# Kernel tuning notes

Measured on AMD Instinct MI355X. Metric: run time of the kernel, lower is better.

## Reference

```python
import jax, jax.numpy as jnp
import numpy as np

N = 8192      # atoms
B = 64        # molecules
E = 262144    # edges
S = 4         # species
NMAX = 8      # radial basis size
CUT = 5.0     # cutoff radius
AVG_ATOMS = 128.0
E_SCALE = 1.0
PS_DIM = (S * NMAX) ** 2 * 4  # l_max=3 -> 4 l channels -> 4096
H1, H2 = 1024, 1024
OUT = 1


def _sph_harm(u):
    # real spherical harmonics up to l=3, input unit vectors [E,3] -> [E,16]
    x, y, z = u[:, 0], u[:, 1], u[:, 2]
    x2, y2, z2 = x * x, y * y, z * z
    return jnp.stack([
        0.28209479 * jnp.ones_like(x),
        0.48860251 * y, 0.48860251 * z, 0.48860251 * x,
        1.09254843 * x * y, 1.09254843 * y * z, 0.31539157 * (3.0 * z2 - 1.0),
        1.09254843 * x * z, 0.54627422 * (x2 - y2),
        0.59004359 * y * (3.0 * x2 - y2), 2.89061144 * x * y * z,
        0.45704579 * y * (5.0 * z2 - 1.0), 0.37317633 * z * (5.0 * z2 - 3.0),
        0.45704579 * x * (5.0 * z2 - 1.0), 1.44530572 * z * (x2 - y2),
        0.59004359 * x * (x2 - 3.0 * y2),
    ], axis=-1)


def setup_inputs() -> dict:
    key = jax.random.key(0)
    ks = jax.random.split(key, 12)
    positions = jax.random.normal(ks[0], (N, 3), dtype=jnp.float32) * 1.5  # dense cloud so many pairs < CUT
    cells = jnp.tile(20.0 * jnp.eye(3, dtype=jnp.float32)[None], (B, 1, 1))
    numbers = jax.random.randint(ks[1], (N,), 0, S)
    edge_indices = jax.random.randint(ks[2], (2, E), 0, N)
    edge_offsets = jnp.zeros((E, 3), dtype=jnp.float32)
    batch = jnp.arange(N) // (N // B)
    gamma = 1.0 + 0.1 * jax.random.normal(ks[3], (PS_DIM,), dtype=jnp.float32)
    beta = 0.1 * jax.random.normal(ks[4], (PS_DIM,), dtype=jnp.float32)
    W_ps = jax.random.normal(ks[5], (PS_DIM, OUT), dtype=jnp.float32) / np.sqrt(PS_DIM)
    W1 = jax.random.normal(ks[6], (PS_DIM, H1), dtype=jnp.float32) / np.sqrt(PS_DIM)
    W2 = jax.random.normal(ks[7], (H1, H2), dtype=jnp.float32) / np.sqrt(H1)
    W3 = jax.random.normal(ks[8], (H2, OUT), dtype=jnp.float32) / np.sqrt(H2)
    W_comp = jax.random.normal(ks[9], (S, OUT), dtype=jnp.float32) / np.sqrt(S)
    return dict(positions=positions, cells=cells, numbers=numbers,
                edge_indices=edge_indices, edge_offsets=edge_offsets, batch=batch,
                gamma=gamma, beta=beta, W_ps=W_ps, W1=W1, W2=W2, W3=W3, W_comp=W_comp)


def reference(positions, cells, numbers, edge_indices, edge_offsets, batch,
              gamma, beta, W_ps, W1, W2, W3, W_comp):
    i, j = edge_indices[0], edge_indices[1]  # center, neighbor
    # periodic shift: fractional offsets through the cell of the center's molecule
    shift = jnp.einsum('ec,ecd->ed', edge_offsets, cells[batch[i]])
    rvec = positions[j] - positions[i] + shift                      # [E,3]
    r = jnp.sqrt(jnp.sum(rvec * rvec, axis=-1) + 1e-12)             # [E]
    u = rvec / r[:, None]
    fc = 0.5 * (jnp.cos(jnp.pi * jnp.minimum(r, CUT) / CUT) + 1.0) * (r < CUT)
    n = jnp.arange(1, NMAX + 1, dtype=positions.dtype)
    R = fc[:, None] * jnp.sin(jnp.pi * n[None, :] * r[:, None] / CUT) / r[:, None]  # [E,NMAX]
    Y = _sph_harm(u)                                                # [E,16]
    edge_feat = R[:, :, None] * Y[:, None, :]                       # [E,NMAX,16]
    # spherical expansion c[i, species(j), n, lm] via scatter-add
    seg = i * S + numbers[j]
    c = jax.ops.segment_sum(edge_feat, seg, num_segments=N * S)     # [N*S,NMAX,16]
    c = c.reshape(N, S * NMAX, 16)
    # power spectrum: contract over m within each l block
    bounds = [(0, 1), (1, 4), (4, 9), (9, 16)]
    p = [jnp.einsum('ixm,iym->ixy', c[:, :, s:e], c[:, :, s:e]) for s, e in bounds]
    ps = jnp.stack(p, axis=-1).reshape(N, PS_DIM)                   # [N,4096]
    # LayerNorm (eps=1e-5, affine)
    mu = jnp.mean(ps, axis=-1, keepdims=True)
    var = jnp.var(ps, axis=-1, keepdims=True)
    psn = (ps - mu) / jnp.sqrt(var + 1e-5) * gamma + beta
    # linear branch + MLP branch
    psl = psn @ W_ps                                                # [N,1]
    h = jax.nn.silu(psn @ W1)
    h = jax.nn.silu(h @ W2)
    psnn = h @ W3                                                   # [N,1]
    # pool atomic energies into per-molecule totals (index_add)
    energies = jax.ops.segment_sum(psl + psnn, batch, num_segments=B) / AVG_ATOMS
    # eval path: composition baseline
    comp = jax.ops.segment_sum(jax.nn.one_hot(numbers, S, dtype=psn.dtype), batch, num_segments=B)
    return energies * E_SCALE + comp @ W_comp                       # [B,1]
```

## Files before the change

### kernel.cpp

```cpp
#include <hip/hip_runtime.h>
#include <hip/hip_bf16.h>
#include <math.h>

#define N_ATOMS 8192
#define B_BATCH 64
#define E_EDGES 262144
#define S_SPEC 4
#define NMAX 8
#define PS_DIM 4096
#define PS_K 2304
#define H1_DIM 1024
#define CAP4 48
#define CUTR 5.0f
#define PI_F 3.14159265358979f

typedef float floatx4 __attribute__((ext_vector_type(4)));
typedef int intx8 __attribute__((ext_vector_type(8)));
typedef unsigned char u8;

__device__ __forceinline__ void g2lds16(const void* g, void* l) {
    __builtin_amdgcn_global_load_lds(
        (const __attribute__((address_space(1))) void*)g,
        (__attribute__((address_space(3))) void*)l, 16, 0, 0);
}

__device__ __forceinline__ int pk_fp8x4(float a, float b, float c, float d) {
    int lo = __builtin_amdgcn_cvt_pk_fp8_f32(a, b, 0, false);
    return __builtin_amdgcn_cvt_pk_fp8_f32(c, d, lo, true);
}

__global__ __launch_bounds__(256) void prep_kernel(
    const float* __restrict__ pos, const float* __restrict__ cells,
    const int* __restrict__ numbers, const int* __restrict__ ei,
    const float* __restrict__ eo, const int* __restrict__ batch,
    int* __restrict__ cnt, float4* __restrict__ bucket,
    const float* __restrict__ W1, const float* __restrict__ gamma,
    const float* __restrict__ beta, const float* __restrict__ Wps,
    const float* __restrict__ W2,
    u8* __restrict__ Wt1, u8* __restrict__ Wt2, float* __restrict__ b1,
    float* __restrict__ gw, float* __restrict__ S23, float* __restrict__ out)
{
    if (blockIdx.x < 512) {
        if (blockIdx.x == 0 && threadIdx.x < B_BATCH) out[threadIdx.x] = 0.0f;
        int e0 = blockIdx.x * 512 + threadIdx.x;
        int e1 = e0 + 256;
        int i0 = ei[e0],            i1 = ei[e1];
        int j0 = ei[E_EDGES + e0],  j1 = ei[E_EDGES + e1];
        int bb0 = batch[i0],        bb1 = batch[i1];
        int sp0 = numbers[j0],      sp1 = numbers[j1];
        float o00 = eo[e0 * 3 + 0], o01 = eo[e0 * 3 + 1], o02 = eo[e0 * 3 + 2];
        float o10 = eo[e1 * 3 + 0], o11 = eo[e1 * 3 + 1], o12 = eo[e1 * 3 + 2];
        const float* c0 = cells + bb0 * 9;
        const float* c1 = cells + bb1 * 9;
        float rv0[3], rv1[3];
        #pragma unroll
        for (int d = 0; d < 3; ++d) {
            float sh0 = o00 * c0[0 * 3 + d] + o01 * c0[1 * 3 + d] + o02 * c0[2 * 3 + d];
            float sh1 = o10 * c1[0 * 3 + d] + o11 * c1[1 * 3 + d] + o12 * c1[2 * 3 + d];
            rv0[d] = pos[j0 * 3 + d] - pos[i0 * 3 + d] + sh0;
            rv1[d] = pos[j1 * 3 + d] - pos[i1 * 3 + d] + sh1;
        }
        float r20 = rv0[0] * rv0[0] + rv0[1] * rv0[1] + rv0[2] * rv0[2] + 1e-12f;
        float r21 = rv1[0] * rv1[0] + rv1[1] * rv1[1] + rv1[2] * rv1[2] + 1e-12f;
        if (r20 < CUTR * CUTR) {
            float a1 = sqrtf(r20) * (PI_F / CUTR);
            int q = i0 * S_SPEC + sp0;
            int slot = atomicAdd(&cnt[q], 1);
            if (slot < CAP4)
                bucket[q * CAP4 + slot] = make_float4(rv0[0], rv0[1], rv0[2], a1);
        }
        if (r21 < CUTR * CUTR) {
            float a1 = sqrtf(r21) * (PI_F / CUTR);
            int q = i1 * S_SPEC + sp1;
            int slot = atomicAdd(&cnt[q], 1);
            if (slot < CAP4)
                bucket[q * CAP4 + slot] = make_float4(rv1[0], rv1[1], rv1[2], a1);
        }
        return;
    }

    if (blockIdx.x == 3840) {
        __shared__ float rs[8][2];
        int t = threadIdx.x, lane = t & 63, wv = t >> 6;
        float s2 = 0.0f, s3 = 0.0f;
        #pragma unroll
        for (int it = 0; it < 4; ++it) {
            int p4 = it * 256 + t;
            float4 g = *(const float4*)(gamma + p4 * 4);
            float4 bt = *(const float4*)(beta + p4 * 4);
            float4 w = *(const float4*)(Wps + p4 * 4);
            float4 gwv = make_float4(g.x * w.x, g.y * w.y, g.z * w.z, g.w * w.w);
            *(float4*)(gw + p4 * 4) = gwv;
            s2 += gwv.x + gwv.y + gwv.z + gwv.w;
            s3 += bt.x * w.x + bt.y * w.y + bt.z * w.z + bt.w * w.w;
        }
        #pragma unroll
        for (int o = 32; o > 0; o >>= 1) {
            s2 += __shfl_down(s2, o);
            s3 += __shfl_down(s3, o);
        }
        if (lane == 0) { rs[wv][0] = s2; rs[wv][1] = s3; }
        __syncthreads();
        if (t == 0) {
            S23[0] = rs[0][0] + rs[1][0] + rs[2][0] + rs[3][0];
            S23[1] = rs[0][1] + rs[1][1] + rs[2][1] + rs[3][1];
        }
        return;
    }

    __shared__ float tbuf[32][33];
    __shared__ float bred[8][32];
    int wid = blockIdx.x - 512;
    int by = wid & 31;
    int bx = wid >> 5;
    int tx = threadIdx.x & 31, ty = threadIdx.x >> 5;
    int n0 = by * 32;

    if (bx < 72) {
        int k0 = bx * 32;
        float bacc = 0.0f;
        for (int r = 0; r < 32; r += 8) {
            int kk = ty + r;
            int kp = k0 + kk;
            int u = kp >> 2, lb = kp & 3;
            float val = 0.0f;
            if (u < 528) {
                int x = 0;
                while ((x + 1) * (64 - x) / 2 <= u) ++x;
                int y = x + (u - x * (65 - x) / 2);
                int p1 = x * 128 + y * 4 + lb;
                float w1v = W1[(size_t)p1 * H1_DIM + n0 + tx];
                val = gamma[p1] * w1v;
                bacc += beta[p1] * w1v;
                if (x < y) {
                    int p2 = y * 128 + x * 4 + lb;
                    float w2v = W1[(size_t)p2 * H1_DIM + n0 + tx];
                    val += gamma[p2] * w2v;
                    bacc += beta[p2] * w2v;
                }
            }
            tbuf[kk][tx] = val;
        }
        bred[ty][tx] = bacc;
        __syncthreads();
        if (ty == 0) {
            float s = 0.0f;
            #pragma unroll
            for (int i = 0; i < 8; ++i) s += bred[i][tx];
            atomicAdd(&b1[n0 + tx], s);
        }
        if (threadIdx.x < 64) {
            int nl = threadIdx.x >> 1, cc = threadIdx.x & 1;
            int n = n0 + nl;
            unsigned int w[4];
            #pragma unroll
            for (int g = 0; g < 4; ++g) {
                int kb = cc * 16 + g * 4;
                w[g] = (unsigned int)pk_fp8x4(
                    tbuf[kb + 0][nl] * 64.0f, tbuf[kb + 1][nl] * 64.0f,
                    tbuf[kb + 2][nl] * 64.0f, tbuf[kb + 3][nl] * 64.0f);
            }
            int gc = (k0 >> 4) + cc;
            int gcs = (gc & ~7) | ((gc & 7) ^ (n & 7));
            *(uint4*)(Wt1 + (size_t)n * PS_K + (size_t)gcs * 16) =
                make_uint4(w[0], w[1], w[2], w[3]);
        }
    } else {
        int k0 = (bx - 72) * 32;
        #pragma unroll
        for (int r = 0; r < 32; r += 8)
            tbuf[ty + r][tx] = W2[(size_t)(k0 + ty + r) * H1_DIM + n0 + tx];
        __syncthreads();
        if (threadIdx.x < 64) {
            int nl = threadIdx.x >> 1, cc = threadIdx.x & 1;
            int n = n0 + nl;
            unsigned int w[4];
            #pragma unroll
            for (int g = 0; g < 4; ++g) {
                int kb = cc * 16 + g * 4;
                w[g] = (unsigned int)pk_fp8x4(
                    tbuf[kb + 0][nl] * 32.0f, tbuf[kb + 1][nl] * 32.0f,
                    tbuf[kb + 2][nl] * 32.0f, tbuf[kb + 3][nl] * 32.0f);
            }
            int gc = (k0 >> 4) + cc;
            int gcs = (gc & ~7) | ((gc & 7) ^ (n & 7));
            *(uint4*)(Wt2 + (size_t)n * H1_DIM + (size_t)gcs * 16) =
                make_uint4(w[0], w[1], w[2], w[3]);
        }
    }
}

__global__ __launch_bounds__(256) void accum_ps_kernel(
    const float4* __restrict__ bucket, const int* __restrict__ cnt,
    const float* __restrict__ gw, const float* __restrict__ S23,
    u8* __restrict__ psn, float* __restrict__ psl)
{
    __shared__ __align__(16) float cl[4][32 * 20];
    __shared__ __align__(16) u8 ps_s8[PS_K];
    __shared__ float red[12];

    int t = threadIdx.x;
    int wv = t >> 6, lane = t & 63;
    int atom0 = blockIdx.x * 4;

    {
        int atom = atom0 + wv;
        int sp_l = lane >> 4;
        int nidx = (lane >> 1) & 7;
        float nf = (float)(nidx + 1);
        int par = lane & 1;

        int myCnt = cnt[atom * S_SPEC + sp_l];
        if (myCnt > CAP4) myCnt = CAP4;
        int m1 = max(myCnt, __shfl_xor(myCnt, 16));
        int mx = max(m1, __shfl_xor(m1, 32));

        const float4* q = bucket + (size_t)(atom * S_SPEC + sp_l) * CAP4;
        float acc[8] = {};
        #pragma unroll 2
        for (int e = 0; e < mx; ++e) {
            float4 d = q[e];
            bool valid = e < myCnt;
            float a1 = d.w;
            float inv_r = (PI_F / CUTR) * __frcp_rn(a1);
            float fc = 0.5f * __cosf(a1) + 0.5f;
            float rn = fc * inv_r * __sinf(nf * a1);
            rn = valid ? rn : 0.0f;

            float x = d.x * inv_r, y = d.y * inv_r, z = d.z * inv_r;
            float x2 = x * x, y2 = y * y, z2 = z * z;
            float Ys[8];
            if (par == 0) {
                Ys[0] = 0.28209479f;
                Ys[1] = 0.48860251f * y;
                Ys[2] = 0.48860251f * z;
                Ys[3] = 0.48860251f * x;
                Ys[4] = 1.09254843f * x * y;
                Ys[5] = 1.09254843f * y * z;
                Ys[6] = 0.31539157f * (3.0f * z2 - 1.0f);
                Ys[7] = 1.09254843f * x * z;
            } else {
                Ys[0] = 0.54627422f * (x2 - y2);
                Ys[1] = 0.59004359f * y * (3.0f * x2 - y2);
                Ys[2] = 2.89061144f * x * y * z;
                Ys[3] = 0.45704579f * y * (5.0f * z2 - 1.0f);
                Ys[4] = 0.37317633f * z * (5.0f * z2 - 3.0f);
                Ys[5] = 0.45704579f * x * (5.0f * z2 - 1.0f);
                Ys[6] = 1.44530572f * z * (x2 - y2);
                Ys[7] = 0.59004359f * x * (x2 - 3.0f * y2);
            }
            #pragma unroll
            for (int k = 0; k < 8; ++k) acc[k] += rn * Ys[k];
        }
        int X = sp_l * 8 + nidx;
        float* dst = &cl[wv][X * 20 + par * 8];
        *(float4*)(dst + 0) = make_float4(acc[0], acc[1], acc[2], acc[3]);
        *(float4*)(dst + 4) = make_float4(acc[4], acc[5], acc[6], acc[7]);
    }
    if (t < 48) ((int*)ps_s8)[528 + t] = 0;
    __syncthreads();

    float S2c = S23[0], S3c = S23[1];

    for (int a = 0; a < 4; ++a) {
        int atom = atom0 + a;
        const float* cl_x = cl[a];

        int y = t & 31;
        int xb = t >> 5;
        float4 cya = *(const float4*)&cl_x[y * 20 + 0];
        float4 cyb = *(const float4*)&cl_x[y * 20 + 4];
        float4 cyc = *(const float4*)&cl_x[y * 20 + 8];
        float4 cyd = *(const float4*)&cl_x[y * 20 + 12];

        float ps[4][4];
        float sum = 0.0f, sumsq = 0.0f, S1 = 0.0f;
        #pragma unroll
        for (int q = 0; q < 4; ++q) {
            int x = xb + 8 * q;
            float4 xa = *(const float4*)&cl_x[x * 20 + 0];
            float4 xbv = *(const float4*)&cl_x[x * 20 + 4];
            float4 xc = *(const float4*)&cl_x[x * 20 + 8];
            float4 xd = *(const float4*)&cl_x[x * 20 + 12];
            float s0 = xa.x * cya.x;
            float s1 = xa.y * cya.y + xa.z * cya.z + xa.w * cya.w;
            float s2 = xbv.x * cyb.x + xbv.y * cyb.y + xbv.z * cyb.z + xbv.w * cyb.w
                     + xc.x * cyc.x;
            float s3 = xc.y * cyc.y + xc.z * cyc.z + xc.w * cyc.w
                     + xd.x * cyd.x + xd.y * cyd.y + xd.z * cyd.z + xd.w * cyd.w;
            ps[q][0] = s0; ps[q][1] = s1; ps[q][2] = s2; ps[q][3] = s3;
            sum += s0 + s1 + s2 + s3;
            sumsq += s0 * s0 + s1 * s1 + s2 * s2 + s3 * s3;
            int p = t + 256 * q;
            float4 gwv = *(const float4*)(gw + p * 4);
            S1 += s0 * gwv.x + s1 * gwv.y + s2 * gwv.z + s3 * gwv.w;
        }
        #pragma unroll
        for (int o = 32; o > 0; o >>= 1) {
            sum += __shfl_down(sum, o);
            sumsq += __shfl_down(sumsq, o);
            S1 += __shfl_down(S1, o);
        }
        if ((t & 63) == 0) { red[wv] = sum; red[4 + wv] = sumsq; red[8 + wv] = S1; }
        __syncthreads();
        float tot = red[0] + red[1] + red[2] + red[3];
        float totsq = red[4] + red[5] + red[6] + red[7];
        float S1t = red[8] + red[9] + red[10] + red[11];
        float mu = tot * (1.0f / PS_DIM);
        float var = totsq * (1.0f / PS_DIM) - mu * mu;
        float inv = rsqrtf(var + 1e-5f);
        if (t == 0) psl[atom] = inv * (S1t - mu * S2c) + S3c;

        #pragma unroll
        for (int q = 0; q < 4; ++q) {
            int p = t + 256 * q;
            float z0 = (ps[q][0] - mu) * inv;
            float z1 = (ps[q][1] - mu) * inv;
            float z2 = (ps[q][2] - mu) * inv;
            float z3 = (ps[q][3] - mu) * inv;
            int x = p >> 5, yy = p & 31;
            if (x <= yy) {
                int u = x * (65 - x) / 2 + (yy - x);
                ((int*)ps_s8)[u] = pk_fp8x4(z0, z1, z2, z3);
            }
        }
        __syncthreads();
        u8* rowp = psn + (size_t)atom * PS_K;
        if (t < PS_K / 16) {
            int gcs = (t & ~7) | ((t & 7) ^ (atom & 7));
            *(uint4*)(rowp + (size_t)gcs * 16) = *(const uint4*)(ps_s8 + (size_t)t * 16);
        }
    }
}

__global__ __launch_bounds__(256) void gemm_f8_kernel(
    const u8* __restrict__ A, const u8* __restrict__ Bt,
    u8* __restrict__ H, const float* __restrict__ b1,
    int M, int Nc, int K, float invs)
{
    __shared__ __align__(16) char smem[65536];
    int tid = threadIdx.x;
    int bm = blockIdx.x, bn = blockIdx.y;
    int wave = tid >> 6, lane = tid & 63;
    int wm = (wave >> 1) * 64, wn = (wave & 1) * 64;
    int lm = lane & 15, quad = lane >> 4;

    floatx4 acc[4][4] = {};
    const int rowA0 = bm * 128, rowB0 = bn * 128;
    const size_t stride = (size_t)K;
    const char* Ab = (const char*)A + (size_t)rowA0 * stride;
    const char* Bb = (const char*)Bt + (size_t)rowB0 * stride;
    const int sA = 0x7F7F7F7F, sB = 0x7F7F7F7F;

    for (int k0 = 0; k0 < K; k0 += 256) {
        #pragma unroll
        for (int s = 0; s < 8; ++s) {
            int L = s * 256 + tid;
            int row = L >> 4, boff = (L & 15) * 16;
            int lbase = (s * 256 + wave * 64) * 16;
            g2lds16(Ab + (size_t)row * stride + k0 + boff, smem + lbase);
        }
        #pragma unroll
        for (int s = 0; s < 8; ++s) {
            int L = s * 256 + tid;
            int row = L >> 4, boff = (L & 15) * 16;
            int lbase = (s * 256 + wave * 64) * 16;
            g2lds16(Bb + (size_t)row * stride + k0 + boff, smem + 32768 + lbase);
        }
        __syncthreads();
        int key = lm & 7;
        int c0 = (2 * quad) ^ key, c1 = (2 * quad + 1) ^ key;
        #pragma unroll
        for (int h = 0; h < 2; ++h) {
            intx8 af[4], bfr[4];
            #pragma unroll
            for (int mi = 0; mi < 4; ++mi) {
                const char* base = smem + (wm + mi * 16 + lm) * 256 + h * 128;
                uint4 lo = *(const uint4*)(base + c0 * 16);
                uint4 hi = *(const uint4*)(base + c1 * 16);
                af[mi][0] = lo.x; af[mi][1] = lo.y; af[mi][2] = lo.z; af[mi][3] = lo.w;
                af[mi][4] = hi.x; af[mi][5] = hi.y; af[mi][6] = hi.z; af[mi][7] = hi.w;
            }
            #pragma unroll
            for (int ni = 0; ni < 4; ++ni) {
                const char* base = smem + 32768 + (wn + ni * 16 + lm) * 256 + h * 128;
                uint4 lo = *(const uint4*)(base + c0 * 16);
                uint4 hi = *(const uint4*)(base + c1 * 16);
                bfr[ni][0] = lo.x; bfr[ni][1] = lo.y; bfr[ni][2] = lo.z; bfr[ni][3] = lo.w;
                bfr[ni][4] = hi.x; bfr[ni][5] = hi.y; bfr[ni][6] = hi.z; bfr[ni][7] = hi.w;
            }
            #pragma unroll
            for (int mi = 0; mi < 4; ++mi)
                #pragma unroll
                for (int ni = 0; ni < 4; ++ni)
                    acc[mi][ni] = __builtin_amdgcn_mfma_scale_f32_16x16x128_f8f6f4(
                        af[mi], bfr[ni], acc[mi][ni], 0, 0, 0, sA, 0, sB);
        }
        __syncthreads();
    }

    u8* Cs8 = (u8*)smem;
    #pragma unroll
    for (int mi = 0; mi < 4; ++mi)
        #pragma unroll
        for (int ni = 0; ni < 4; ++ni) {
            float bv = b1[bn * 128 + wn + ni * 16 + lm];
            #pragma unroll
            for (int r = 0; r < 4; ++r) {
                int row = wm + mi * 16 + quad * 4 + r;
                int col = wn + ni * 16 + lm;
                float v = acc[mi][ni][r] * invs + bv;
                v = v / (1.0f + __expf(-v));
                int pk = __builtin_amdgcn_cvt_pk_fp8_f32(v, 0.0f, 0, false);
                Cs8[row * 128 + col] = (u8)(pk & 0xFF);
            }
        }
    __syncthreads();
    #pragma unroll
    for (int c2 = 0; c2 < 4; ++c2) {
        int L = c2 * 256 + tid;
        int row = L >> 3, cc = L & 7;
        int gcs = cc ^ (row & 7);
        *(uint4*)(H + (size_t)(rowA0 + row) * Nc + (size_t)(bn * 8 + gcs) * 16) =
            *(const uint4*)(Cs8 + (size_t)L * 16);
    }
}

__global__ __launch_bounds__(256) void gemm2_fused_kernel(
    const u8* __restrict__ A, const u8* __restrict__ Bt,
    const float* __restrict__ W3, const float* __restrict__ psl,
    const int* __restrict__ numbers, const float* __restrict__ Wcomp,
    float* __restrict__ out, int Nc, int K, float invs)
{
    __shared__ __align__(16) char smem[65536];
    int tid = threadIdx.x;
    int bm = blockIdx.x, bn = blockIdx.y;
    int wave = tid >> 6, lane = tid & 63;
    int wm = (wave >> 1) * 64, wn = (wave & 1) * 64;
    int lm = lane & 15, quad = lane >> 4;

    floatx4 acc[4][4] = {};
    const int rowA0 = bm * 128, rowB0 = bn * 128;
    const size_t stride = (size_t)K;
    const char* Ab = (const char*)A + (size_t)rowA0 * stride;
    const char* Bb = (const char*)Bt + (size_t)rowB0 * stride;
    const int sA = 0x7F7F7F7F, sB = 0x7F7F7F7F;

    for (int k0 = 0; k0 < K; k0 += 256) {
        #pragma unroll
        for (int s = 0; s < 8; ++s) {
            int L = s * 256 + tid;
            int row = L >> 4, boff = (L & 15) * 16;
            int lbase = (s * 256 + wave * 64) * 16;
            g2lds16(Ab + (size_t)row * stride + k0 + boff, smem + lbase);
        }
        #pragma unroll
        for (int s = 0; s < 8; ++s) {
            int L = s * 256 + tid;
            int row = L >> 4, boff = (L & 15) * 16;
            int lbase = (s * 256 + wave * 64) * 16;
            g2lds16(Bb + (size_t)row * stride + k0 + boff, smem + 32768 + lbase);
        }
        __syncthreads();
        int key = lm & 7;
        int c0 = (2 * quad) ^ key, c1 = (2 * quad + 1) ^ key;
        #pragma unroll
        for (int h = 0; h < 2; ++h) {
            intx8 af[4], bfr[4];
            #pragma unroll
            for (int mi = 0; mi < 4; ++mi) {
                const char* base = smem + (wm + mi * 16 + lm) * 256 + h * 128;
                uint4 lo = *(const uint4*)(base + c0 * 16);
                uint4 hi = *(const uint4*)(base + c1 * 16);
                af[mi][0] = lo.x; af[mi][1] = lo.y; af[mi][2] = lo.z; af[mi][3] = lo.w;
                af[mi][4] = hi.x; af[mi][5] = hi.y; af[mi][6] = hi.z; af[mi][7] = hi.w;
            }
            #pragma unroll
            for (int ni = 0; ni < 4; ++ni) {
                const char* base = smem + 32768 + (wn + ni * 16 + lm) * 256 + h * 128;
                uint4 lo = *(const uint4*)(base + c0 * 16);
                uint4 hi = *(const uint4*)(base + c1 * 16);
                bfr[ni][0] = lo.x; bfr[ni][1] = lo.y; bfr[ni][2] = lo.z; bfr[ni][3] = lo.w;
                bfr[ni][4] = hi.x; bfr[ni][5] = hi.y; bfr[ni][6] = hi.z; bfr[ni][7] = hi.w;
            }
            #pragma unroll
            for (int mi = 0; mi < 4; ++mi)
                #pragma unroll
                for (int ni = 0; ni < 4; ++ni)
                    acc[mi][ni] = __builtin_amdgcn_mfma_scale_f32_16x16x128_f8f6f4(
                        af[mi], bfr[ni], acc[mi][ni], 0, 0, 0, sA, 0, sB);
        }
        __syncthreads();
    }

    float lt = 0.0f;
    #pragma unroll
    for (int ni = 0; ni < 4; ++ni) {
        float w3v = W3[bn * 128 + wn + ni * 16 + lm];
        #pragma unroll
        for (int mi = 0; mi < 4; ++mi)
            #pragma unroll
            for (int r = 0; r < 4; ++r) {
                float v = acc[mi][ni][r] * invs;
                v = v / (1.0f + __expf(-v));
                lt += v * w3v;
            }
    }
    #pragma unroll
    for (int o = 32; o > 0; o >>= 1) lt += __shfl_down(lt, o);
    float* wsum = (float*)smem;
    int* c4 = ((int*)smem) + 8;
    float* shp = ((float*)smem) + 12;
    if (tid < S_SPEC) c4[tid] = 0;
    if (lane == 0) wsum[wave] = lt;
    __syncthreads();
    if (tid == 0)
        atomicAdd(&out[bm],
                  (wsum[0] + wsum[1] + wsum[2] + wsum[3]) * (1.0f / 128.0f));
    if (bn == 0) {
        if (tid < 128) {
            int a = bm * 128 + tid;
            float e = psl[a];
            atomicAdd(&c4[numbers[a]], 1);
            #pragma unroll
            for (int o = 32; o > 0; o >>= 1) e += __shfl_down(e, o);
            if ((tid & 63) == 0) shp[tid >> 6] = e;
        }
        __syncthreads();
        if (tid == 0) {
            float r = (shp[0] + shp[1]) * (1.0f / 128.0f);
            #pragma unroll
            for (int s = 0; s < S_SPEC; ++s) r += (float)c4[s] * Wcomp[s];
            atomicAdd(&out[bm], r);
        }
    }
}

extern "C" void kernel_launch(void* const* d_in, const int* in_sizes, int n_in,
                              void* d_out, int out_size, void* d_ws, size_t ws_size,
                              hipStream_t stream)
{
    const float* positions = (const float*)d_in[0];
    const float* cells     = (const float*)d_in[1];
    const int*   numbers   = (const int*)d_in[2];
    const int*   ei        = (const int*)d_in[3];
    const float* eo        = (const float*)d_in[4];
    const int*   batch     = (const int*)d_in[5];
    const float* gamma     = (const float*)d_in[6];
    const float* beta      = (const float*)d_in[7];
    const float* W_ps      = (const float*)d_in[8];
    const float* W1        = (const float*)d_in[9];
    const float* W2        = (const float*)d_in[10];
    const float* W3        = (const float*)d_in[11];
    const float* W_comp    = (const float*)d_in[12];
    float* out = (float*)d_out;

    char* ws = (char*)d_ws;
    float4* bucket = (float4*)ws;  ws += (size_t)N_ATOMS * S_SPEC * CAP4 * 16;
    u8*    psn  = (u8*)ws;     ws += (size_t)N_ATOMS * PS_K;
    u8*    h1   = (u8*)ws;     ws += (size_t)N_ATOMS * H1_DIM;
    u8*    Wt1  = (u8*)ws;     ws += (size_t)H1_DIM * PS_K;
    u8*    Wt2  = (u8*)ws;     ws += (size_t)H1_DIM * H1_DIM;
    float* psl  = (float*)ws;  ws += (size_t)N_ATOMS * 4;
    int*   cnt  = (int*)ws;    ws += (size_t)N_ATOMS * S_SPEC * 4;
    float* b1   = (float*)ws;  ws += (size_t)H1_DIM * 4;
    float* gw   = (float*)ws;  ws += (size_t)PS_DIM * 4;
    float* S23  = (float*)ws;  ws += 2 * 4;

    hipMemsetAsync(cnt, 0, (N_ATOMS * S_SPEC + H1_DIM) * sizeof(int), stream);

    prep_kernel<<<3841, 256, 0, stream>>>(
        positions, cells, numbers, ei, eo, batch, cnt, bucket,
        W1, gamma, beta, W_ps, W2, Wt1, Wt2, b1, gw, S23, out);

    accum_ps_kernel<<<N_ATOMS / 4, 256, 0, stream>>>(
        bucket, cnt, gw, S23, psn, psl);

    gemm_f8_kernel<<<dim3(N_ATOMS / 128, H1_DIM / 128), 256, 0, stream>>>(
        psn, Wt1, h1, b1, N_ATOMS, H1_DIM, PS_K, 1.0f / 64.0f);

    gemm2_fused_kernel<<<dim3(N_ATOMS / 128, H1_DIM / 128), 256, 0, stream>>>(
        h1, Wt2, W3, psl, numbers, W_comp, out, H1_DIM, H1_DIM, 1.0f / 32.0f);
}
```

Measured before the change: 182.3 us.

## Shrink first FP8 GEMM tile to 64x128 with smaller K-step

Restructures the first FP8 MFMA GEMM from 128x128 block tiles with a 256-byte K-step into 64x128 tiles with a 128-byte K-step. Each wave now owns 16 rows and 8 column tiles instead of a 64x64 sub-tile. LDS use drops from 64 KiB to 24 KiB and the grid doubles, which should raise occupancy and spread work across more CUs. The cost is less operand reuse per loaded byte (more B traffic) and twice as many barriers per unit of K work.

```diff
diff --git a/kernel.cpp b/kernel.cpp
--- a/kernel.cpp
+++ b/kernel.cpp
@@ -338,87 +338,79 @@
     u8* __restrict__ H, const float* __restrict__ b1,
     int M, int Nc, int K, float invs)
 {
-    __shared__ __align__(16) char smem[65536];
+    __shared__ __align__(16) char smem[24576];
     int tid = threadIdx.x;
     int bm = blockIdx.x, bn = blockIdx.y;
     int wave = tid >> 6, lane = tid & 63;
-    int wm = (wave >> 1) * 64, wn = (wave & 1) * 64;
+    int wm = wave * 16;
     int lm = lane & 15, quad = lane >> 4;
 
-    floatx4 acc[4][4] = {};
-    const int rowA0 = bm * 128, rowB0 = bn * 128;
+    floatx4 acc[8] = {};
+    const int rowA0 = bm * 64, rowB0 = bn * 128;
     const size_t stride = (size_t)K;
     const char* Ab = (const char*)A + (size_t)rowA0 * stride;
     const char* Bb = (const char*)Bt + (size_t)rowB0 * stride;
     const int sA = 0x7F7F7F7F, sB = 0x7F7F7F7F;
 
-    for (int k0 = 0; k0 < K; k0 += 256) {
-        #pragma unroll
-        for (int s = 0; s < 8; ++s) {
+    int key = lm & 7;
+    int c0 = (2 * quad) ^ key, c1 = (2 * quad + 1) ^ key;
+
+    for (int k0 = 0; k0 < K; k0 += 128) {
+        #pragma unroll
+        for (int s = 0; s < 2; ++s) {
             int L = s * 256 + tid;
-            int row = L >> 4, boff = (L & 15) * 16;
+            int row = L >> 3, boff = (L & 7) * 16;
             int lbase = (s * 256 + wave * 64) * 16;
             g2lds16(Ab + (size_t)row * stride + k0 + boff, smem + lbase);
         }
         #pragma unroll
-        for (int s = 0; s < 8; ++s) {
+        for (int s = 0; s < 4; ++s) {
             int L = s * 256 + tid;
-            int row = L >> 4, boff = (L & 15) * 16;
+            int row = L >> 3, boff = (L & 7) * 16;
             int lbase = (s * 256 + wave * 64) * 16;
-            g2lds16(Bb + (size_t)row * stride + k0 + boff, smem + 32768 + lbase);
-        }
-        __syncthreads();
-        int key = lm & 7;
-        int c0 = (2 * quad) ^ key, c1 = (2 * quad + 1) ^ key;
-        #pragma unroll
-        for (int h = 0; h < 2; ++h) {
-            intx8 af[4], bfr[4];
-            #pragma unroll
-            for (int mi = 0; mi < 4; ++mi) {
-                const char* base = smem + (wm + mi * 16 + lm) * 256 + h * 128;
-                uint4 lo = *(const uint4*)(base + c0 * 16);
-                uint4 hi = *(const uint4*)(base + c1 * 16);
-                af[mi][0] = lo.x; af[mi][1] = lo.y; af[mi][2] = lo.z; af[mi][3] = lo.w;
-                af[mi][4] = hi.x; af[mi][5] = hi.y; af[mi][6] = hi.z; af[mi][7] = hi.w;
-            }
-            #pragma unroll
-            for (int ni = 0; ni < 4; ++ni) {
-                const char* base = smem + 32768 + (wn + ni * 16 + lm) * 256 + h * 128;
-                uint4 lo = *(const uint4*)(base + c0 * 16);
-                uint4 hi = *(const uint4*)(base + c1 * 16);
-                bfr[ni][0] = lo.x; bfr[ni][1] = lo.y; bfr[ni][2] = lo.z; bfr[ni][3] = lo.w;
-                bfr[ni][4] = hi.x; bfr[ni][5] = hi.y; bfr[ni][6] = hi.z; bfr[ni][7] = hi.w;
-            }
-            #pragma unroll
-            for (int mi = 0; mi < 4; ++mi)
-                #pragma unroll
-                for (int ni = 0; ni < 4; ++ni)
-                    acc[mi][ni] = __builtin_amdgcn_mfma_scale_f32_16x16x128_f8f6f4(
-                        af[mi], bfr[ni], acc[mi][ni], 0, 0, 0, sA, 0, sB);
+            g2lds16(Bb + (size_t)row * stride + k0 + boff, smem + 8192 + lbase);
+        }
+        __syncthreads();
+        intx8 af;
+        {
+            const char* base = smem + (wm + lm) * 128;
+            uint4 lo = *(const uint4*)(base + c0 * 16);
+            uint4 hi = *(const uint4*)(base + c1 * 16);
+            af[0] = lo.x; af[1] = lo.y; af[2] = lo.z; af[3] = lo.w;
+            af[4] = hi.x; af[5] = hi.y; af[6] = hi.z; af[7] = hi.w;
+        }
+        #pragma unroll
+        for (int ni = 0; ni < 8; ++ni) {
+            intx8 bfr;
+            const char* base = smem + 8192 + (ni * 16 + lm) * 128;
+            uint4 lo = *(const uint4*)(base + c0 * 16);
+            uint4 hi = *(const uint4*)(base + c1 * 16);
+            bfr[0] = lo.x; bfr[1] = lo.y; bfr[2] = lo.z; bfr[3] = lo.w;
+            bfr[4] = hi.x; bfr[5] = hi.y; bfr[6] = hi.z; bfr[7] = hi.w;
+            acc[ni] = __builtin_amdgcn_mfma_scale_f32_16x16x128_f8f6f4(
+                af, bfr, acc[ni], 0, 0, 0, sA, 0, sB);
         }
         __syncthreads();
     }
 
     u8* Cs8 = (u8*)smem;
     #pragma unroll
-    for (int mi = 0; mi < 4; ++mi)
-        #pragma unroll
-        for (int ni = 0; ni < 4; ++ni) {
-            float bv = b1[bn * 128 + wn + ni * 16 + lm];
-            #pragma unroll
-            for (int r = 0; r < 4; ++r) {
-                int row = wm + mi * 16 + quad * 4 + r;
-                int col = wn + ni * 16 + lm;
-                float v = acc[mi][ni][r] * invs + bv;
-                v = v / (1.0f + __expf(-v));
-                int pk = __builtin_amdgcn_cvt_pk_fp8_f32(v, 0.0f, 0, false);
-                Cs8[row * 128 + col] = (u8)(pk & 0xFF);
-            }
-        }
+    for (int ni = 0; ni < 8; ++ni) {
+        float bv = b1[bn * 128 + ni * 16 + lm];
+        #pragma unroll
+        for (int r = 0; r < 4; ++r) {
+            int row = wm + quad * 4 + r;
+            int col = ni * 16 + lm;
+            float v = acc[ni][r] * invs + bv;
+            v = v / (1.0f + __expf(-v));
+            int pk = __builtin_amdgcn_cvt_pk_fp8_f32(v, 0.0f, 0, false);
+            Cs8[row * 128 + col] = (u8)(pk & 0xFF);
+        }
+    }
     __syncthreads();
     #pragma unroll
-    for (int c2 = 0; c2 < 4; ++c2) {
-        int L = c2 * 256 + tid;
+    for (int s = 0; s < 2; ++s) {
+        int L = s * 256 + tid;
         int row = L >> 3, cc = L & 7;
         int gcs = cc ^ (row & 7);
         *(uint4*)(H + (size_t)(rowA0 + row) * Nc + (size_t)(bn * 8 + gcs) * 16) =
@@ -576,7 +568,7 @@
     accum_ps_kernel<<<N_ATOMS / 4, 256, 0, stream>>>(
         bucket, cnt, gw, S23, psn, psl);
 
-    gemm_f8_kernel<<<dim3(N_ATOMS / 128, H1_DIM / 128), 256, 0, stream>>>(
+    gemm_f8_kernel<<<dim3(N_ATOMS / 64, H1_DIM / 128), 256, 0, stream>>>(
         psn, Wt1, h1, b1, N_ATOMS, H1_DIM, PS_K, 1.0f / 64.0f);
 
     gemm2_fused_kernel<<<dim3(N_ATOMS / 128, H1_DIM / 128), 256, 0, stream>>>(
```

New measurement: 188.8 us. +3.5%, slower.
